# Optimization experiments

Measured on AMD Instinct MI355X. Metric: run time of the kernel, lower is better.

## Reference

```python
import jax, jax.numpy as jnp
import numpy as np

N = 262144          # ray samples
L = 16              # grid levels
T = 2 ** 19         # hash table entries per level
F = 2               # features per entry
NMIN, NMAX = 16, 2048
SB = 1.0            # scene_bound
DW, CW = 64, 64     # density / color MLP widths

_PRIMES = jnp.array([1, 2654435761, 805459861], dtype=jnp.uint32)
_OFFS = jnp.asarray(np.stack(np.meshgrid([0, 1], [0, 1], [0, 1], indexing='ij'), -1).reshape(8, 3), dtype=jnp.uint32)  # 8 cube corners


def _scalings():
    g = np.exp((np.log(NMAX) - np.log(NMIN)) / (L - 1))
    return jnp.asarray(np.floor(NMIN * g ** np.arange(L)), dtype=jnp.float32)  # (L,)


def hash_encode(pos01, table):
    # pos01: (N,3) in [0,1]; table: (L*T, F)
    scaled = pos01[:, None, :] * _scalings()[None, :, None]        # (N,L,3)
    floor = jnp.floor(scaled)
    frac = scaled - floor                                          # (N,L,3)
    corners = floor.astype(jnp.uint32)[:, :, None, :] + _OFFS[None, None]  # (N,L,8,3)
    h = corners * _PRIMES                                          # uint32 wraparound hashing
    idx = (h[..., 0] ^ h[..., 1] ^ h[..., 2]) % jnp.uint32(T)      # (N,L,8)
    idx = idx.astype(jnp.int32) + (jnp.arange(L, dtype=jnp.int32) * T)[None, :, None]
    feats = table[idx]                                             # (N,L,8,F) gather
    sel = _OFFS.astype(bool)[None, None]                           # (1,1,8,3)
    w = jnp.prod(jnp.where(sel, frac[:, :, None, :], 1.0 - frac[:, :, None, :]), axis=-1)  # (N,L,8)
    out = jnp.einsum('nlcf,nlc->nlf', feats, w)                    # trilinear interp
    return out.reshape(out.shape[0], L * F)                        # (N, 32)


def sh_encode(d):
    # 4th-order real spherical harmonics, 16 components (instant-ngp convention)
    x, y, z = d[..., 0], d[..., 1], d[..., 2]
    xx, yy, zz = x * x, y * y, z * z
    xy, yz, xz = x * y, y * z, x * z
    return jnp.stack([
        jnp.full_like(x, 0.28209479177387814),
        -0.48860251190291987 * y,
        0.48860251190291987 * z,
        -0.48860251190291987 * x,
        1.0925484305920792 * xy,
        -1.0925484305920792 * yz,
        0.94617469575755997 * zz - 0.31539156525252005,
        -1.0925484305920792 * xz,
        0.54627421529603959 * (xx - yy),
        0.59004358992664352 * y * (-3.0 * xx + yy),
        2.8906114426405538 * xy * z,
        0.45704579946446572 * y * (1.0 - 5.0 * zz),
        0.3731763325901154 * z * (5.0 * zz - 3.0),
        0.45704579946446572 * x * (1.0 - 5.0 * zz),
        1.445305721320277 * z * (xx - yy),
        0.59004358992664352 * x * (xx - 3.0 * yy),
    ], axis=-1)  # (N,16)


def setup_inputs() -> dict:
    key = jax.random.key(0)
    ks = jax.random.split(key, 10)
    position = jax.random.uniform(ks[0], (N, 3), jnp.float32, -SB, SB)
    d = jax.random.normal(ks[1], (N, 3), jnp.float32)
    direction = d / jnp.linalg.norm(d, axis=-1, keepdims=True)
    hash_table = jax.random.uniform(ks[2], (L * T, F), jnp.float32, -1e-4, 1e-4)
    def dense(k, fin, fout, std):
        return (jax.random.normal(k, (fin, fout), jnp.float32) * std,
                jnp.zeros((fout,), jnp.float32))
    w1, b1 = dense(ks[3], L * F, DW, 0.01)      # normal() init in source
    w2, b2 = dense(ks[4], DW, 16, 0.01)
    w3, b3 = dense(ks[5], 16 + 16, CW, 0.01)
    w4, b4 = dense(ks[6], CW, CW, 0.01)
    w5, b5 = dense(ks[7], CW, 3, 0.1)           # default lecun-ish scale
    return dict(position=position, direction=direction, hash_table=hash_table,
                w1=w1, b1=b1, w2=w2, b2=b2, w3=w3, b3=b3, w4=w4, b4=b4, w5=w5, b5=b5)


def reference(position, direction, hash_table, w1, b1, w2, b2, w3, b3, w4, b4, w5, b5):
    p = (position + SB) / (2.0 * SB)                 # -> [0,1]
    enc = hash_encode(p, hash_table)                 # (N,32)
    h = jax.nn.relu(enc @ w1 + b1)                   # density MLP
    h = h @ w2 + b2                                  # (N,16)
    density = jnp.exp(h[:, 0:1])                     # exponential_density_activation
    sh = sh_encode(direction)                        # (N,16)
    c = jnp.concatenate([h, sh], axis=-1)            # (N,32)
    c = jax.nn.relu(c @ w3 + b3)
    c = jax.nn.relu(c @ w4 + b4)
    c = c @ w5 + b5
    color = jax.nn.sigmoid(c)                        # high_dynamic_range=False
    return jnp.concatenate([density, color], axis=-1)  # (N,4) drgbs
```

## Files before the change

### kernel.cpp

```cpp
#include <hip/hip_runtime.h>
#include <cmath>

namespace {
constexpr int kN = 262144;
constexpr int kL = 16;
constexpr int kT = 1 << 19;
constexpr unsigned kTMask = kT - 1;

typedef __attribute__((ext_vector_type(8))) short short8;
typedef __attribute__((ext_vector_type(4))) float f32x4;
typedef __attribute__((ext_vector_type(4))) unsigned short ushort4v;

struct Scales { float s[kL]; };

__device__ __forceinline__ unsigned short f2bf(float f) {
    unsigned u = __builtin_bit_cast(unsigned, f);
    return (unsigned short)((u + 0x7FFFu + ((u >> 16) & 1u)) >> 16);
}

__global__ __launch_bounds__(256) void prep_w(
    const float* __restrict__ w1, const float* __restrict__ w2,
    const float* __restrict__ w3, const float* __restrict__ w4,
    const float* __restrict__ w5, unsigned short* __restrict__ out)
{
    const int i = blockIdx.x * 256 + threadIdx.x;
    const int f = i >> 9;
    const int l = (i >> 3) & 63;
    const int e = i & 7;
    const int cl = l & 15;
    const int kg = l >> 4;
    float v = 0.0f;
    if (f < 4) {
        v = w1[(kg * 8 + e) * 64 + f * 16 + cl];
    } else if (f < 6) {
        const int q = f - 4;
        v = w2[(q * 32 + kg * 8 + e) * 16 + cl];
    } else if (f < 10) {
        v = w3[(kg * 8 + e) * 64 + (f - 6) * 16 + cl];
    } else if (f < 18) {
        const int g = f - 10, q = g >> 2, nt = g & 3;
        v = w4[(q * 32 + kg * 8 + e) * 64 + nt * 16 + cl];
    } else {
        const int q = f - 18;
        v = (cl < 3) ? w5[(q * 32 + kg * 8 + e) * 3 + cl] : 0.0f;
    }
    out[i] = f2bf(v);
}

__global__ __launch_bounds__(256) void ngp_encode(
    const float* __restrict__ pos,
    const float2* __restrict__ table,
    unsigned* __restrict__ enc,
    Scales sc)
{
    const int bid = blockIdx.x;
    const int xcd = bid & 7;
    const int l = xcd + ((bid >> 12) << 3);
    const int chunk = (bid >> 3) & 511;
    const int n0 = (chunk << 9) | threadIdx.x;

    const float s = sc.s[l];
    const float2* __restrict__ tl = table + (size_t)l * kT;

    float2 f[2][8];
    float rx[2], ry[2], rz[2];

    #pragma unroll
    for (int t = 0; t < 2; ++t) {
        const int n = n0 + t * 256;
        const float px = (__builtin_nontemporal_load(&pos[n * 3 + 0]) + 1.0f) * 0.5f;
        const float py = (__builtin_nontemporal_load(&pos[n * 3 + 1]) + 1.0f) * 0.5f;
        const float pz = (__builtin_nontemporal_load(&pos[n * 3 + 2]) + 1.0f) * 0.5f;
        const float sx = px * s, sy = py * s, sz = pz * s;
        const float fx = floorf(sx), fy = floorf(sy), fz = floorf(sz);
        rx[t] = sx - fx; ry[t] = sy - fy; rz[t] = sz - fz;
        const unsigned cx = (unsigned)fx, cy = (unsigned)fy, cz = (unsigned)fz;
        const unsigned hy0 = cy * 2654435761u, hy1 = (cy + 1u) * 2654435761u;
        const unsigned hz0 = cz * 805459861u,  hz1 = (cz + 1u) * 805459861u;
        #pragma unroll
        for (int c = 0; c < 8; ++c) {
            const unsigned ox = (c >> 2) & 1u, oy = (c >> 1) & 1u, oz = c & 1u;
            const unsigned h = (cx + ox) ^ (oy ? hy1 : hy0) ^ (oz ? hz1 : hz0);
            f[t][c] = tl[h & kTMask];
        }
    }

    #pragma unroll
    for (int t = 0; t < 2; ++t) {
        float f0 = 0.f, f1 = 0.f;
        #pragma unroll
        for (int c = 0; c < 8; ++c) {
            const unsigned ox = (c >> 2) & 1u, oy = (c >> 1) & 1u, oz = c & 1u;
            const float w = (ox ? rx[t] : 1.f - rx[t]) * (oy ? ry[t] : 1.f - ry[t]) * (oz ? rz[t] : 1.f - rz[t]);
            f0 = fmaf(f[t][c].x, w, f0);
            f1 = fmaf(f[t][c].y, w, f1);
        }
        const unsigned packed = (unsigned)f2bf(f0) | ((unsigned)f2bf(f1) << 16);
        __builtin_nontemporal_store(packed, &enc[(size_t)l * kN + (n0 + t * 256)]);
    }
}

__global__ __launch_bounds__(256) void ngp_mlp_mfma(
    const unsigned* __restrict__ enc,
    const unsigned short* __restrict__ wbf,
    const float* __restrict__ dir,
    const float* __restrict__ b1, const float* __restrict__ b2,
    const float* __restrict__ b3, const float* __restrict__ b4,
    const float* __restrict__ b5,
    float* __restrict__ out)
{
    __shared__ unsigned short sA[4][4096];
    __shared__ unsigned short sB[4][2048];

    const int tid = threadIdx.x;
    const int wid = tid >> 6;
    const int l   = tid & 63;
    const int cl  = l & 15;
    const int kg  = l >> 4;
    unsigned short* __restrict__ A_ = sA[wid];
    unsigned short* __restrict__ B_ = sB[wid];
    const int gbase = blockIdx.x * 256 + wid * 64;

    {
        const int s = gbase + l;
        const float x = dir[s * 3 + 0], y = dir[s * 3 + 1], z = dir[s * 3 + 2];
        const float xx = x * x, yy = y * y, zz = z * z;
        const float xy = x * y, yz = y * z, xz = x * z;
        float sh[16];
        sh[0] = 0.28209479177387814f;
        sh[1] = -0.48860251190291987f * y;
        sh[2] = 0.48860251190291987f * z;
        sh[3] = -0.48860251190291987f * x;
        sh[4] = 1.0925484305920792f * xy;
        sh[5] = -1.0925484305920792f * yz;
        sh[6] = 0.94617469575755997f * zz - 0.31539156525252005f;
        sh[7] = -1.0925484305920792f * xz;
        sh[8] = 0.54627421529603959f * (xx - yy);
        sh[9] = 0.59004358992664352f * y * (-3.0f * xx + yy);
        sh[10] = 2.8906114426405538f * xy * z;
        sh[11] = 0.45704579946446572f * y * (1.0f - 5.0f * zz);
        sh[12] = 0.3731763325901154f * z * (5.0f * zz - 3.0f);
        sh[13] = 0.45704579946446572f * x * (1.0f - 5.0f * zz);
        sh[14] = 1.445305721320277f * z * (xx - yy);
        sh[15] = 0.59004358992664352f * x * (xx - 3.0f * yy);
        #pragma unroll
        for (int j = 0; j < 16; ++j)
            B_[(l >> 4) * 512 + (16 + j) * 16 + (l & 15)] = f2bf(sh[j]);
    }

    short8 A1[4];
    #pragma unroll
    for (int m = 0; m < 4; ++m) {
        #pragma unroll
        for (int j = 0; j < 4; ++j) {
            const unsigned v = enc[(size_t)(kg * 4 + j) * kN + (gbase + m * 16 + cl)];
            A1[m][2 * j]     = (short)(v & 0xFFFFu);
            A1[m][2 * j + 1] = (short)(v >> 16);
        }
    }
    {
        short8 B1[4];
        #pragma unroll
        for (int nt = 0; nt < 4; ++nt)
            B1[nt] = *reinterpret_cast<const short8*>(&wbf[(size_t)(nt) * 512 + l * 8]);

        f32x4 acc[4][4];
        #pragma unroll
        for (int nt = 0; nt < 4; ++nt) {
            const float bv = b1[nt * 16 + cl];
            #pragma unroll
            for (int m = 0; m < 4; ++m) {
                acc[m][nt][0] = bv; acc[m][nt][1] = bv; acc[m][nt][2] = bv; acc[m][nt][3] = bv;
            }
        }
        #pragma unroll
        for (int m = 0; m < 4; ++m)
            #pragma unroll
            for (int nt = 0; nt < 4; ++nt)
                acc[m][nt] = __builtin_amdgcn_mfma_f32_16x16x32_bf16(A1[m], B1[nt], acc[m][nt], 0, 0, 0);

        #pragma unroll
        for (int m = 0; m < 4; ++m) {
            #pragma unroll
            for (int nt = 0; nt < 4; ++nt) {
                ushort4v pk;
                #pragma unroll
                for (int r = 0; r < 4; ++r) pk[r] = f2bf(fmaxf(acc[m][nt][r], 0.0f));
                *reinterpret_cast<ushort4v*>(&A_[m * 1024 + (nt * 16 + cl) * 16 + kg * 4]) = pk;
            }
        }
    }

    {
        short8 A2[4][2];
        #pragma unroll
        for (int m = 0; m < 4; ++m)
            #pragma unroll
            for (int q = 0; q < 2; ++q)
                #pragma unroll
                for (int e = 0; e < 8; ++e)
                    A2[m][q][e] = (short)A_[m * 1024 + (q * 32 + kg * 8 + e) * 16 + cl];

        short8 B2[2];
        #pragma unroll
        for (int q = 0; q < 2; ++q)
            B2[q] = *reinterpret_cast<const short8*>(&wbf[(size_t)(4 + q) * 512 + l * 8]);

        f32x4 acc[4];
        const float bv = b2[cl];
        #pragma unroll
        for (int m = 0; m < 4; ++m) { acc[m][0] = bv; acc[m][1] = bv; acc[m][2] = bv; acc[m][3] = bv; }
        #pragma unroll
        for (int m = 0; m < 4; ++m)
            #pragma unroll
            for (int q = 0; q < 2; ++q)
                acc[m] = __builtin_amdgcn_mfma_f32_16x16x32_bf16(A2[m][q], B2[q], acc[m], 0, 0, 0);

        #pragma unroll
        for (int m = 0; m < 4; ++m) {
            if (cl == 0) {
                #pragma unroll
                for (int r = 0; r < 4; ++r)
                    out[(size_t)(gbase + m * 16 + kg * 4 + r) * 4 + 0] = expf(acc[m][r]);
            }
            ushort4v pk;
            #pragma unroll
            for (int r = 0; r < 4; ++r) pk[r] = f2bf(acc[m][r]);
            *reinterpret_cast<ushort4v*>(&B_[m * 512 + cl * 16 + kg * 4]) = pk;
        }
    }

    {
        short8 A3[4];
        #pragma unroll
        for (int m = 0; m < 4; ++m)
            #pragma unroll
            for (int e = 0; e < 8; ++e)
                A3[m][e] = (short)B_[m * 512 + (kg * 8 + e) * 16 + cl];

        short8 B3[4];
        #pragma unroll
        for (int nt = 0; nt < 4; ++nt)
            B3[nt] = *reinterpret_cast<const short8*>(&wbf[(size_t)(6 + nt) * 512 + l * 8]);

        f32x4 acc[4][4];
        #pragma unroll
        for (int nt = 0; nt < 4; ++nt) {
            const float bv = b3[nt * 16 + cl];
            #pragma unroll
            for (int m = 0; m < 4; ++m) {
                acc[m][nt][0] = bv; acc[m][nt][1] = bv; acc[m][nt][2] = bv; acc[m][nt][3] = bv;
            }
        }
        #pragma unroll
        for (int m = 0; m < 4; ++m)
            #pragma unroll
            for (int nt = 0; nt < 4; ++nt)
                acc[m][nt] = __builtin_amdgcn_mfma_f32_16x16x32_bf16(A3[m], B3[nt], acc[m][nt], 0, 0, 0);

        #pragma unroll
        for (int m = 0; m < 4; ++m) {
            #pragma unroll
            for (int nt = 0; nt < 4; ++nt) {
                ushort4v pk;
                #pragma unroll
                for (int r = 0; r < 4; ++r) pk[r] = f2bf(fmaxf(acc[m][nt][r], 0.0f));
                *reinterpret_cast<ushort4v*>(&A_[m * 1024 + (nt * 16 + cl) * 16 + kg * 4]) = pk;
            }
        }
    }

    {
        short8 A4[4][2];
        #pragma unroll
        for (int m = 0; m < 4; ++m)
            #pragma unroll
            for (int q = 0; q < 2; ++q)
                #pragma unroll
                for (int e = 0; e < 8; ++e)
                    A4[m][q][e] = (short)A_[m * 1024 + (q * 32 + kg * 8 + e) * 16 + cl];

        short8 B4[2][4];
        #pragma unroll
        for (int q = 0; q < 2; ++q)
            #pragma unroll
            for (int nt = 0; nt < 4; ++nt)
                B4[q][nt] = *reinterpret_cast<const short8*>(&wbf[(size_t)(10 + q * 4 + nt) * 512 + l * 8]);

        f32x4 acc[4][4];
        #pragma unroll
        for (int nt = 0; nt < 4; ++nt) {
            const float bv = b4[nt * 16 + cl];
            #pragma unroll
            for (int m = 0; m < 4; ++m) {
                acc[m][nt][0] = bv; acc[m][nt][1] = bv; acc[m][nt][2] = bv; acc[m][nt][3] = bv;
            }
        }
        #pragma unroll
        for (int m = 0; m < 4; ++m)
            #pragma unroll
            for (int nt = 0; nt < 4; ++nt)
                #pragma unroll
                for (int q = 0; q < 2; ++q)
                    acc[m][nt] = __builtin_amdgcn_mfma_f32_16x16x32_bf16(A4[m][q], B4[q][nt], acc[m][nt], 0, 0, 0);

        #pragma unroll
        for (int m = 0; m < 4; ++m) {
            #pragma unroll
            for (int nt = 0; nt < 4; ++nt) {
                ushort4v pk;
                #pragma unroll
                for (int r = 0; r < 4; ++r) pk[r] = f2bf(fmaxf(acc[m][nt][r], 0.0f));
                *reinterpret_cast<ushort4v*>(&A_[m * 1024 + (nt * 16 + cl) * 16 + kg * 4]) = pk;
            }
        }
    }

    {
        short8 A5[4][2];
        #pragma unroll
        for (int m = 0; m < 4; ++m)
            #pragma unroll
            for (int q = 0; q < 2; ++q)
                #pragma unroll
                for (int e = 0; e < 8; ++e)
                    A5[m][q][e] = (short)A_[m * 1024 + (q * 32 + kg * 8 + e) * 16 + cl];

        short8 B5[2];
        #pragma unroll
        for (int q = 0; q < 2; ++q)
            B5[q] = *reinterpret_cast<const short8*>(&wbf[(size_t)(18 + q) * 512 + l * 8]);

        f32x4 acc[4];
        const float bv = (cl < 3) ? b5[cl] : 0.0f;
        #pragma unroll
        for (int m = 0; m < 4; ++m) { acc[m][0] = bv; acc[m][1] = bv; acc[m][2] = bv; acc[m][3] = bv; }
        #pragma unroll
        for (int m = 0; m < 4; ++m)
            #pragma unroll
            for (int q = 0; q < 2; ++q)
                acc[m] = __builtin_amdgcn_mfma_f32_16x16x32_bf16(A5[m][q], B5[q], acc[m], 0, 0, 0);

        if (cl < 3) {
            #pragma unroll
            for (int m = 0; m < 4; ++m)
                #pragma unroll
                for (int r = 0; r < 4; ++r)
                    out[(size_t)(gbase + m * 16 + kg * 4 + r) * 4 + 1 + cl] =
                        1.0f / (1.0f + expf(-acc[m][r]));
        }
    }
}

}

extern "C" void kernel_launch(void* const* d_in, const int* in_sizes, int n_in,
                              void* d_out, int out_size, void* d_ws, size_t ws_size,
                              hipStream_t stream) {
    (void)in_sizes; (void)n_in; (void)out_size; (void)ws_size;

    Scales sc;
    const double g = exp((log(2048.0) - log(16.0)) / 15.0);
    for (int l = 0; l < kL; ++l) sc.s[l] = (float)floor(16.0 * pow(g, (double)l));

    const float*  pos   = (const float*)d_in[0];
    const float*  dir   = (const float*)d_in[1];
    const float2* table = (const float2*)d_in[2];
    const float *w1 = (const float*)d_in[3],  *b1 = (const float*)d_in[4];
    const float *w2 = (const float*)d_in[5],  *b2 = (const float*)d_in[6];
    const float *w3 = (const float*)d_in[7],  *b3 = (const float*)d_in[8];
    const float *w4 = (const float*)d_in[9],  *b4 = (const float*)d_in[10];
    const float *w5 = (const float*)d_in[11], *b5 = (const float*)d_in[12];
    float* out = (float*)d_out;

    unsigned short* wbf = (unsigned short*)d_ws;
    unsigned* enc = (unsigned*)((char*)d_ws + 32768);

    prep_w<<<40, 256, 0, stream>>>(w1, w2, w3, w4, w5, wbf);
    ngp_encode<<<8192, 256, 0, stream>>>(pos, table, enc, sc);
    ngp_mlp_mfma<<<kN / 256, 256, 0, stream>>>(enc, wbf, dir,
        b1, b2, b3, b4, b5, out);
}
```

Baseline: 177.0 us.

## Pair x-adjacent hash corners into one 16-byte gather when x is even

The encode kernel exploits the fact that corners differing only in x+1 hash to adjacent table slots when cx is even (XOR with cx vs cx+1 flips only bit 0). Each of the four yz-corner pairs is now fetched with one aligned float4 load, and a second set of four float2 loads is issued only when cx is odd. The block-to-level mapping is also simplified, dropping the XCD-interleaved layout, and the nontemporal load and store hints are removed. This is meant to cut gather transactions, at the cost of a divergent extra load path for about half the lanes and possibly worse L2 locality per level.

```diff
diff --git a/kernel.cpp b/kernel.cpp
--- a/kernel.cpp
+++ b/kernel.cpp
@@ -54,49 +54,73 @@
     Scales sc)
 {
     const int bid = blockIdx.x;
-    const int xcd = bid & 7;
-    const int l = xcd + ((bid >> 12) << 3);
-    const int chunk = (bid >> 3) & 511;
-    const int n0 = (chunk << 9) | threadIdx.x;
+    const int l = bid >> 9;
+    const int n0 = ((bid & 511) << 9) | threadIdx.x;
 
     const float s = sc.s[l];
     const float2* __restrict__ tl = table + (size_t)l * kT;
 
-    float2 f[2][8];
+    float4 pr[2][4];
+    float2 ex[2][4];
+    unsigned idx0v[2][4];
+    unsigned hyzv[2][4];
+    unsigned cxv[2];
     float rx[2], ry[2], rz[2];
 
     #pragma unroll
     for (int t = 0; t < 2; ++t) {
         const int n = n0 + t * 256;
-        const float px = (__builtin_nontemporal_load(&pos[n * 3 + 0]) + 1.0f) * 0.5f;
-        const float py = (__builtin_nontemporal_load(&pos[n * 3 + 1]) + 1.0f) * 0.5f;
-        const float pz = (__builtin_nontemporal_load(&pos[n * 3 + 2]) + 1.0f) * 0.5f;
+        const float px = (pos[n * 3 + 0] + 1.0f) * 0.5f;
+        const float py = (pos[n * 3 + 1] + 1.0f) * 0.5f;
+        const float pz = (pos[n * 3 + 2] + 1.0f) * 0.5f;
         const float sx = px * s, sy = py * s, sz = pz * s;
         const float fx = floorf(sx), fy = floorf(sy), fz = floorf(sz);
         rx[t] = sx - fx; ry[t] = sy - fy; rz[t] = sz - fz;
         const unsigned cx = (unsigned)fx, cy = (unsigned)fy, cz = (unsigned)fz;
+        cxv[t] = cx;
         const unsigned hy0 = cy * 2654435761u, hy1 = (cy + 1u) * 2654435761u;
         const unsigned hz0 = cz * 805459861u,  hz1 = (cz + 1u) * 805459861u;
         #pragma unroll
-        for (int c = 0; c < 8; ++c) {
-            const unsigned ox = (c >> 2) & 1u, oy = (c >> 1) & 1u, oz = c & 1u;
-            const unsigned h = (cx + ox) ^ (oy ? hy1 : hy0) ^ (oz ? hz1 : hz0);
-            f[t][c] = tl[h & kTMask];
+        for (int j = 0; j < 4; ++j) {
+            const unsigned hyz = ((j >> 1) ? hy1 : hy0) ^ ((j & 1) ? hz1 : hz0);
+            hyzv[t][j] = hyz;
+            const unsigned idx0 = (cx ^ hyz) & kTMask;
+            idx0v[t][j] = idx0;
+            pr[t][j] = *reinterpret_cast<const float4*>(tl + (idx0 & ~1u));
         }
     }
 
     #pragma unroll
     for (int t = 0; t < 2; ++t) {
+        if (cxv[t] & 1u) {
+            const unsigned cx1 = cxv[t] + 1u;
+            #pragma unroll
+            for (int j = 0; j < 4; ++j)
+                ex[t][j] = tl[(cx1 ^ hyzv[t][j]) & kTMask];
+        }
+    }
+
+    #pragma unroll
+    for (int t = 0; t < 2; ++t) {
+        const bool odd = (cxv[t] & 1u) != 0u;
+        const float wx0 = 1.0f - rx[t], wx1 = rx[t];
         float f0 = 0.f, f1 = 0.f;
         #pragma unroll
-        for (int c = 0; c < 8; ++c) {
-            const unsigned ox = (c >> 2) & 1u, oy = (c >> 1) & 1u, oz = c & 1u;
-            const float w = (ox ? rx[t] : 1.f - rx[t]) * (oy ? ry[t] : 1.f - ry[t]) * (oz ? rz[t] : 1.f - rz[t]);
-            f0 = fmaf(f[t][c].x, w, f0);
-            f1 = fmaf(f[t][c].y, w, f1);
-        }
-        const unsigned packed = (unsigned)f2bf(f0) | ((unsigned)f2bf(f1) << 16);
-        __builtin_nontemporal_store(packed, &enc[(size_t)l * kN + (n0 + t * 256)]);
+        for (int j = 0; j < 4; ++j) {
+            const float wyz = ((j >> 1) ? ry[t] : 1.0f - ry[t]) *
+                              ((j & 1) ? rz[t] : 1.0f - rz[t]);
+            const bool hi = (idx0v[t][j] & 1u) != 0u;
+            const float c0x = hi ? pr[t][j].z : pr[t][j].x;
+            const float c0y = hi ? pr[t][j].w : pr[t][j].y;
+            const float c1x = odd ? ex[t][j].x : (hi ? pr[t][j].x : pr[t][j].z);
+            const float c1y = odd ? ex[t][j].y : (hi ? pr[t][j].y : pr[t][j].w);
+            f0 = fmaf(c0x, wx0 * wyz, f0);
+            f1 = fmaf(c0y, wx0 * wyz, f1);
+            f0 = fmaf(c1x, wx1 * wyz, f0);
+            f1 = fmaf(c1y, wx1 * wyz, f1);
+        }
+        enc[(size_t)l * kN + (n0 + t * 256)] =
+            (unsigned)f2bf(f0) | ((unsigned)f2bf(f1) << 16);
     }
 }
 
```

Measured after the change: 151.4 us. 14.5% less time.
